# Kernel tuning notes

Measured on AMD Instinct MI355X. Metric: run time of the kernel, lower is better.

Reference implementation:

```python
import jax, jax.numpy as jnp
import numpy as np

N = 50000        # node_num
E = 1600000      # num edges (avg degree 32)
IN_DIM = 128
OUT_DIM = 64
SLOPE = 0.1      # leaky relu slope_ratio
EPS = 1e-12


def setup_inputs() -> dict:
    key = jax.random.key(0)
    k0, k1, k2, k3 = jax.random.split(key, 4)
    x = jax.random.normal(k0, (N, IN_DIM), dtype=jnp.float32)
    edge_index = jax.random.randint(k1, (2, E), 0, N, dtype=jnp.int64)
    # Linear(in_dim, out_dim) params
    W = jax.random.normal(k2, (OUT_DIM, IN_DIM), dtype=jnp.float32) * (1.0 / np.sqrt(IN_DIM))
    b = jnp.zeros((OUT_DIM,), dtype=jnp.float32)
    # attention vector a: [2*out_dim, 1], kaiming-normal-ish init
    a = jax.random.normal(k3, (2 * OUT_DIM, 1), dtype=jnp.float32) * np.sqrt(2.0 / (2 * OUT_DIM))
    return {"x": x, "edge_index": edge_index, "W": W, "b": b, "a": a}


def reference(x, edge_index, W, b, a):
    # new_embeddings = Linear(x)
    new = x @ W.T + b                          # [N, OUT_DIM]
    src = edge_index[0]
    dst = edge_index[1]
    # cat(new[src], new[dst]) @ a  ==  new[src]@a_src + new[dst]@a_dst (avoids [E, 2*OUT] intermediate)
    a_src = a[:OUT_DIM, 0]                     # [OUT_DIM]
    a_dst = a[OUT_DIM:, 0]                     # [OUT_DIM]
    score = new[src] @ a_src + new[dst] @ a_dst  # [E]
    e = jnp.exp(jax.nn.leaky_relu(score, SLOPE))  # [E]
    # spmm(A, ones) -> per-row sum of edge weights; spmm(A, new) -> weighted aggregation
    row_sum = jax.ops.segment_sum(e, src, num_segments=N)                 # [N]
    results = jax.ops.segment_sum(e[:, None] * new[dst], src, num_segments=N)  # [N, OUT_DIM]
    return results / (row_sum[:, None] + EPS)
```

## Files before the change

kernel.cpp:

```cpp
#include <hip/hip_runtime.h>
#include <hip/hip_bf16.h>

#define NN    50000
#define EE    1600000
#define IND   128
#define OUTD  64
#define SLOPE 0.1f

#define BSH    5
#define BW     32
#define NB     1564
#define NFINE  1568
#define CAP    1408
#define CAPT   6
#define CSH    8
#define NC     196
#define CAP1   8832
#define NBLK1  500
#define CHUNK1 (EE / NBLK1)
#define NSPLIT 4
#define SCAP   (CAP1 / NSPLIT)
#define LTILE  64
#define NLIN   782

typedef __attribute__((ext_vector_type(8))) short short8;
typedef __attribute__((ext_vector_type(4))) float float4v;

union SMem {
    struct {
        ushort xs[64 * 136];
        ushort wt[64 * 136];
        float  newt[64 * 68];
    } lin;
    int h[NC];
};

__global__ __launch_bounds__(256) void fused_lincoarse_kernel(
    const float* __restrict__ x, const float* __restrict__ W,
    const float* __restrict__ bias, const float* __restrict__ a,
    const int* __restrict__ ei, int* __restrict__ gcur1,
    unsigned* __restrict__ ebuf1,
    ushort* __restrict__ nbuf2, float* __restrict__ s_src, float* __restrict__ s_dst)
{
    __shared__ SMem sm;
    const int tid = threadIdx.x;

    if (blockIdx.x < NBLK1) {
        int* h = sm.h;
        for (int i = tid; i < NC; i += 256) h[i] = 0;
        __syncthreads();
        const int base = blockIdx.x * CHUNK1;
        const int4* s4p = (const int4*)(ei + base);
        int4 sst[4];
        #pragma unroll
        for (int k = 0; k < 4; ++k) {
            int i = tid + k * 256;
            if (i < CHUNK1 / 4) {
                int4 s4 = s4p[i];
                sst[k] = s4;
                atomicAdd(&h[s4.x >> CSH], 1);
                atomicAdd(&h[s4.y >> CSH], 1);
                atomicAdd(&h[s4.z >> CSH], 1);
                atomicAdd(&h[s4.w >> CSH], 1);
            }
        }
        __syncthreads();
        for (int i = tid; i < NC; i += 256) {
            int c = h[i];
            if (c) h[i] = i * CAP1 + atomicAdd(&gcur1[i * 16], c);
        }
        __syncthreads();
        const int4* d4p = (const int4*)(ei + EE + base);
        #pragma unroll
        for (int k = 0; k < 4; ++k) {
            int i = tid + k * 256;
            if (i < CHUNK1 / 4) {
                int4 s4 = sst[k];
                int4 d4 = d4p[i];
                int p0 = atomicAdd(&h[s4.x >> CSH], 1);
                int p1 = atomicAdd(&h[s4.y >> CSH], 1);
                int p2 = atomicAdd(&h[s4.z >> CSH], 1);
                int p3 = atomicAdd(&h[s4.w >> CSH], 1);
                ebuf1[p0] = ((unsigned)(s4.x & 255) << 16) | (unsigned)d4.x;
                ebuf1[p1] = ((unsigned)(s4.y & 255) << 16) | (unsigned)d4.y;
                ebuf1[p2] = ((unsigned)(s4.z & 255) << 16) | (unsigned)d4.z;
                ebuf1[p3] = ((unsigned)(s4.w & 255) << 16) | (unsigned)d4.w;
            }
        }
        return;
    }

    const int node0 = (blockIdx.x - NBLK1) * LTILE;
    const float4* W4 = (const float4*)W;
    #pragma unroll
    for (int i = 0; i < 8; ++i) {
        int idx = tid + i * 256;
        float4 wv = W4[idx];
        int n = idx >> 5, k = (idx & 31) * 4;
        ushort4 pk; __hip_bfloat16 h;
        h = __float2bfloat16(wv.x); pk.x = *(ushort*)&h;
        h = __float2bfloat16(wv.y); pk.y = *(ushort*)&h;
        h = __float2bfloat16(wv.z); pk.z = *(ushort*)&h;
        h = __float2bfloat16(wv.w); pk.w = *(ushort*)&h;
        *(ushort4*)&sm.lin.wt[n * 136 + k] = pk;
    }
    const float4* x4 = (const float4*)x;
    #pragma unroll
    for (int i = 0; i < 8; ++i) {
        int idx = tid + i * 256;
        int r = idx >> 5, cc = (idx & 31) * 4;
        int gr = node0 + r; if (gr >= NN) gr = NN - 1;
        float4 xv = x4[(size_t)gr * 32 + (idx & 31)];
        ushort4 pk; __hip_bfloat16 h;
        h = __float2bfloat16(xv.x); pk.x = *(ushort*)&h;
        h = __float2bfloat16(xv.y); pk.y = *(ushort*)&h;
        h = __float2bfloat16(xv.z); pk.z = *(ushort*)&h;
        h = __float2bfloat16(xv.w); pk.w = *(ushort*)&h;
        *(ushort4*)&sm.lin.xs[r * 136 + cc] = pk;
    }
    __syncthreads();

    const int w    = tid >> 6;
    const int lane = tid & 63;
    const int q    = lane >> 4;
    const int m16  = lane & 15;
    const float bv = bias[w * 16 + m16];
    #pragma unroll
    for (int t = 0; t < 4; ++t) {
        float4v acc = {0.f, 0.f, 0.f, 0.f};
        #pragma unroll
        for (int kk = 0; kk < IND; kk += 32) {
            short8 af = *(const short8*)&sm.lin.xs[(t * 16 + m16) * 136 + kk + q * 8];
            short8 bf = *(const short8*)&sm.lin.wt[(w * 16 + m16) * 136 + kk + q * 8];
            acc = __builtin_amdgcn_mfma_f32_16x16x32_bf16(af, bf, acc, 0, 0, 0);
        }
        #pragma unroll
        for (int r = 0; r < 4; ++r)
            sm.lin.newt[(t * 16 + q * 4 + r) * 68 + w * 16 + m16] = acc[r] + bv;
    }
    __syncthreads();

    const int jg = tid & 15;
    const int j0 = jg * 4;
    const float a0s = a[j0],        a1s = a[j0 + 1],
                a2s = a[j0 + 2],    a3s = a[j0 + 3];
    const float a0d = a[OUTD + j0],     a1d = a[OUTD + j0 + 1],
                a2d = a[OUTD + j0 + 2], a3d = a[OUTD + j0 + 3];
    #pragma unroll
    for (int t = 0; t < 4; ++t) {
        const int nl = t * 16 + (tid >> 4);
        const int n = node0 + nl;
        float4 va = *(const float4*)&sm.lin.newt[nl * 68 + j0];
        if (n < NN) {
            ushort4 pk; __hip_bfloat16 h;
            h = __float2bfloat16(va.x); pk.x = *(ushort*)&h;
            h = __float2bfloat16(va.y); pk.y = *(ushort*)&h;
            h = __float2bfloat16(va.z); pk.z = *(ushort*)&h;
            h = __float2bfloat16(va.w); pk.w = *(ushort*)&h;
            *(ushort4*)&nbuf2[(size_t)n * OUTD + j0] = pk;
        }
        float ss = va.x * a0s + va.y * a1s + va.z * a2s + va.w * a3s;
        float sd = va.x * a0d + va.y * a1d + va.z * a2d + va.w * a3d;
        #pragma unroll
        for (int m = 1; m < 16; m <<= 1) {
            ss += __shfl_xor(ss, m, 64);
            sd += __shfl_xor(sd, m, 64);
        }
        if (jg == 0 && n < NN) { s_src[n] = ss; s_dst[n] = sd; }
    }
}

__global__ __launch_bounds__(256) void finebin_kernel(
    const unsigned* __restrict__ ebuf1, const int* __restrict__ gcur1,
    int* __restrict__ gcur2, unsigned* __restrict__ ebuf2)
{
    __shared__ unsigned stage[SCAP];
    __shared__ int h[8], lofs[8], grun[8], cur[8];
    const int tid = threadIdx.x;
    const int c   = blockIdx.x >> 2;
    const int sp  = blockIdx.x & 3;
    const int cnt1 = gcur1[c * 16];
    const int seg  = (cnt1 + NSPLIT - 1) / NSPLIT;
    const int lo   = sp * seg;
    const int m    = max(0, min(cnt1, lo + seg) - lo);
    if (tid < 8) h[tid] = 0;
    __syncthreads();
    const unsigned* eb = ebuf1 + (size_t)c * CAP1 + lo;
    for (int i = tid; i < m; i += 256)
        atomicAdd(&h[eb[i] >> 21], 1);
    __syncthreads();
    if (tid == 0) {
        int run = 0;
        #pragma unroll
        for (int f = 0; f < 8; ++f) { lofs[f] = run; run += h[f]; }
    }
    __syncthreads();
    if (tid < 8) {
        cur[tid]  = lofs[tid];
        grun[tid] = atomicAdd(&gcur2[(c * 8 + tid) * 16], h[tid]);
    }
    __syncthreads();
    for (int i = tid; i < m; i += 256) {
        unsigned e = eb[i];
        int pos = atomicAdd(&cur[e >> 21], 1);
        stage[pos] = (((e >> 16) & 31u) << 16) | (e & 0xFFFFu);
    }
    __syncthreads();
    #pragma unroll 1
    for (int f = 0; f < 8; ++f) {
        const int cf = h[f];
        unsigned* dst = ebuf2 + (size_t)(c * 8 + f) * CAP + grun[f];
        const unsigned* sp2 = stage + lofs[f];
        for (int i = tid; i < cf; i += 256) dst[i] = sp2[i];
    }
}

__global__ __launch_bounds__(256) void aggregate_kernel(
    const unsigned* __restrict__ ebuf, const int* __restrict__ gcur,
    const ushort* __restrict__ nbuf2,
    const float* __restrict__ s_src, const float* __restrict__ s_dst,
    float* __restrict__ out)
{
    __shared__ uint2 pairs[CAP];
    __shared__ float ssL[BW];
    __shared__ int cntL[BW], ofs[BW], cur[BW];
    const int tid  = threadIdx.x;
    const int wid  = tid >> 6;
    const int lane = tid & 63;
    const int b    = blockIdx.x;
    const int n0   = b << BSH;
    const uint2* __restrict__ nbufq = (const uint2*)nbuf2;

    if (tid < BW) {
        int n = n0 + tid;
        ssL[tid]  = (n < NN) ? s_src[n] : 0.f;
        cntL[tid] = 0;
    }
    __syncthreads();

    const int cnt = gcur[b * 16];
    const unsigned* eb = ebuf + (size_t)b * CAP;

    unsigned er[CAPT]; float evr[CAPT];
    #pragma unroll
    for (int k = 0; k < CAPT; ++k) {
        int i = tid + k * 256;
        if (i < cnt) {
            unsigned e = eb[i];
            er[k] = e;
            int d  = e & 0xFFFFu;
            int ln = e >> 16;
            float sc = ssL[ln] + s_dst[d];
            float lr = sc > 0.f ? sc : SLOPE * sc;
            evr[k] = __expf(lr);
            atomicAdd(&cntL[ln], 1);
        }
    }
    __syncthreads();

    if (wid == 0) {
        int c = (lane < BW) ? cntL[lane] : 0;
        int sc = c;
        #pragma unroll
        for (int m = 1; m < BW; m <<= 1) {
            int v = __shfl_up(sc, m, 64);
            if (lane >= m) sc += v;
        }
        if (lane < BW) { ofs[lane] = sc - c; cur[lane] = sc - c; }
    }
    __syncthreads();

    #pragma unroll
    for (int k = 0; k < CAPT; ++k) {
        int i = tid + k * 256;
        if (i < cnt) {
            int ln = er[k] >> 16;
            int pos = atomicAdd(&cur[ln], 1);
            pairs[pos] = make_uint2(er[k] & 0xFFFFu, __float_as_uint(evr[k]));
        }
    }
    __syncthreads();

    const int e16 = lane >> 4;
    const int c16 = lane & 15;

    #pragma unroll 1
    for (int t = 0; t < BW / 4; ++t) {
        const int ln  = wid * (BW / 4) + t;
        const int beg = ofs[ln];
        const int len = cntL[ln];

        float a0 = 0.f, a1 = 0.f, a2 = 0.f, a3 = 0.f, es = 0.f;
        int j = 0;
        for (; j + 32 <= len; j += 32) {
            uint2 pA = pairs[beg + j + 0  + e16];
            uint2 pB = pairs[beg + j + 4  + e16];
            uint2 pC = pairs[beg + j + 8  + e16];
            uint2 pD = pairs[beg + j + 12 + e16];
            uint2 pE = pairs[beg + j + 16 + e16];
            uint2 pF = pairs[beg + j + 20 + e16];
            uint2 pG = pairs[beg + j + 24 + e16];
            uint2 pH = pairs[beg + j + 28 + e16];
            uint2 gA = nbufq[pA.x * 16 + c16];
            uint2 gB = nbufq[pB.x * 16 + c16];
            uint2 gC = nbufq[pC.x * 16 + c16];
            uint2 gD = nbufq[pD.x * 16 + c16];
            uint2 gE = nbufq[pE.x * 16 + c16];
            uint2 gF = nbufq[pF.x * 16 + c16];
            uint2 gG = nbufq[pG.x * 16 + c16];
            uint2 gH = nbufq[pH.x * 16 + c16];
            float fA = __uint_as_float(pA.y), fB = __uint_as_float(pB.y);
            float fC = __uint_as_float(pC.y), fD = __uint_as_float(pD.y);
            float fE = __uint_as_float(pE.y), fF = __uint_as_float(pF.y);
            float fG = __uint_as_float(pG.y), fH = __uint_as_float(pH.y);
            es += (fA + fB + fC + fD) + (fE + fF + fG + fH);
            a0 = fmaf(fA, __uint_as_float(gA.x << 16), a0);
            a1 = fmaf(fA, __uint_as_float(gA.x & 0xFFFF0000u), a1);
            a2 = fmaf(fA, __uint_as_float(gA.y << 16), a2);
            a3 = fmaf(fA, __uint_as_float(gA.y & 0xFFFF0000u), a3);
            a0 = fmaf(fB, __uint_as_float(gB.x << 16), a0);
            a1 = fmaf(fB, __uint_as_float(gB.x & 0xFFFF0000u), a1);
            a2 = fmaf(fB, __uint_as_float(gB.y << 16), a2);
            a3 = fmaf(fB, __uint_as_float(gB.y & 0xFFFF0000u), a3);
            a0 = fmaf(fC, __uint_as_float(gC.x << 16), a0);
            a1 = fmaf(fC, __uint_as_float(gC.x & 0xFFFF0000u), a1);
            a2 = fmaf(fC, __uint_as_float(gC.y << 16), a2);
            a3 = fmaf(fC, __uint_as_float(gC.y & 0xFFFF0000u), a3);
            a0 = fmaf(fD, __uint_as_float(gD.x << 16), a0);
            a1 = fmaf(fD, __uint_as_float(gD.x & 0xFFFF0000u), a1);
            a2 = fmaf(fD, __uint_as_float(gD.y << 16), a2);
            a3 = fmaf(fD, __uint_as_float(gD.y & 0xFFFF0000u), a3);
            a0 = fmaf(fE, __uint_as_float(gE.x << 16), a0);
            a1 = fmaf(fE, __uint_as_float(gE.x & 0xFFFF0000u), a1);
            a2 = fmaf(fE, __uint_as_float(gE.y << 16), a2);
            a3 = fmaf(fE, __uint_as_float(gE.y & 0xFFFF0000u), a3);
            a0 = fmaf(fF, __uint_as_float(gF.x << 16), a0);
            a1 = fmaf(fF, __uint_as_float(gF.x & 0xFFFF0000u), a1);
            a2 = fmaf(fF, __uint_as_float(gF.y << 16), a2);
            a3 = fmaf(fF, __uint_as_float(gF.y & 0xFFFF0000u), a3);
            a0 = fmaf(fG, __uint_as_float(gG.x << 16), a0);
            a1 = fmaf(fG, __uint_as_float(gG.x & 0xFFFF0000u), a1);
            a2 = fmaf(fG, __uint_as_float(gG.y << 16), a2);
            a3 = fmaf(fG, __uint_as_float(gG.y & 0xFFFF0000u), a3);
            a0 = fmaf(fH, __uint_as_float(gH.x << 16), a0);
            a1 = fmaf(fH, __uint_as_float(gH.x & 0xFFFF0000u), a1);
            a2 = fmaf(fH, __uint_as_float(gH.y << 16), a2);
            a3 = fmaf(fH, __uint_as_float(gH.y & 0xFFFF0000u), a3);
        }
        for (; j + 16 <= len; j += 16) {
            uint2 pA = pairs[beg + j + 0  + e16];
            uint2 pB = pairs[beg + j + 4  + e16];
            uint2 pC = pairs[beg + j + 8  + e16];
            uint2 pD = pairs[beg + j + 12 + e16];
            uint2 gA = nbufq[pA.x * 16 + c16];
            uint2 gB = nbufq[pB.x * 16 + c16];
            uint2 gC = nbufq[pC.x * 16 + c16];
            uint2 gD = nbufq[pD.x * 16 + c16];
            float fA = __uint_as_float(pA.y), fB = __uint_as_float(pB.y);
            float fC = __uint_as_float(pC.y), fD = __uint_as_float(pD.y);
            es += fA + fB + fC + fD;
            a0 = fmaf(fA, __uint_as_float(gA.x << 16), a0);
            a1 = fmaf(fA, __uint_as_float(gA.x & 0xFFFF0000u), a1);
            a2 = fmaf(fA, __uint_as_float(gA.y << 16), a2);
            a3 = fmaf(fA, __uint_as_float(gA.y & 0xFFFF0000u), a3);
            a0 = fmaf(fB, __uint_as_float(gB.x << 16), a0);
            a1 = fmaf(fB, __uint_as_float(gB.x & 0xFFFF0000u), a1);
            a2 = fmaf(fB, __uint_as_float(gB.y << 16), a2);
            a3 = fmaf(fB, __uint_as_float(gB.y & 0xFFFF0000u), a3);
            a0 = fmaf(fC, __uint_as_float(gC.x << 16), a0);
            a1 = fmaf(fC, __uint_as_float(gC.x & 0xFFFF0000u), a1);
            a2 = fmaf(fC, __uint_as_float(gC.y << 16), a2);
            a3 = fmaf(fC, __uint_as_float(gC.y & 0xFFFF0000u), a3);
            a0 = fmaf(fD, __uint_as_float(gD.x << 16), a0);
            a1 = fmaf(fD, __uint_as_float(gD.x & 0xFFFF0000u), a1);
            a2 = fmaf(fD, __uint_as_float(gD.y << 16), a2);
            a3 = fmaf(fD, __uint_as_float(gD.y & 0xFFFF0000u), a3);
        }
        for (; j < len; j += 4) {
            int idx = j + e16;
            uint2 p = pairs[beg + min(idx, len - 1)];
            float f = (idx < len) ? __uint_as_float(p.y) : 0.f;
            uint2 g = nbufq[p.x * 16 + c16];
            es += f;
            a0 = fmaf(f, __uint_as_float(g.x << 16), a0);
            a1 = fmaf(f, __uint_as_float(g.x & 0xFFFF0000u), a1);
            a2 = fmaf(f, __uint_as_float(g.y << 16), a2);
            a3 = fmaf(f, __uint_as_float(g.y & 0xFFFF0000u), a3);
        }
        es += __shfl_xor(es, 16, 64); es += __shfl_xor(es, 32, 64);
        a0 += __shfl_xor(a0, 16, 64); a0 += __shfl_xor(a0, 32, 64);
        a1 += __shfl_xor(a1, 16, 64); a1 += __shfl_xor(a1, 32, 64);
        a2 += __shfl_xor(a2, 16, 64); a2 += __shfl_xor(a2, 32, 64);
        a3 += __shfl_xor(a3, 16, 64); a3 += __shfl_xor(a3, 32, 64);
        const int n = n0 + ln;
        if (e16 == 0 && n < NN) {
            float inv = 1.f / (es + 1e-12f);
            float4 o = make_float4(a0 * inv, a1 * inv, a2 * inv, a3 * inv);
            *(float4*)&out[(size_t)n * OUTD + c16 * 4] = o;
        }
    }
}

extern "C" void kernel_launch(void* const* d_in, const int* in_sizes, int n_in,
                              void* d_out, int out_size, void* d_ws, size_t ws_size,
                              hipStream_t stream) {
    const float* x  = (const float*)d_in[0];
    const int*   ei = (const int*)d_in[1];
    const float* W  = (const float*)d_in[2];
    const float* b  = (const float*)d_in[3];
    const float* a  = (const float*)d_in[4];
    float* out = (float*)d_out;

    ushort*   nbuf2 = (ushort*)d_ws;
    float*    s_src = (float*)(nbuf2 + (size_t)NN * OUTD);
    float*    s_dst = s_src + NN;
    int*      gcur1 = (int*)(s_dst + NN);
    int*      gcur2 = gcur1 + NC * 16;
    unsigned* ebuf1 = (unsigned*)(gcur2 + NFINE * 16);
    unsigned* ebuf2 = ebuf1 + (size_t)NC * CAP1;

    hipMemsetAsync(gcur1, 0, (NC + NFINE) * 16 * sizeof(int), stream);
    fused_lincoarse_kernel<<<NBLK1 + NLIN, 256, 0, stream>>>(
        x, W, b, a, ei, gcur1, ebuf1, nbuf2, s_src, s_dst);
    finebin_kernel<<<NC * NSPLIT, 256, 0, stream>>>(ebuf1, gcur1, gcur2, ebuf2);
    aggregate_kernel<<<NB, 256, 0, stream>>>(ebuf2, gcur2, nbuf2, s_src, s_dst, out);
    aggregate_kernel<<<NB, 256, 0, stream>>>(ebuf2, gcur2, nbuf2, s_src, s_dst, out);
}
```

Measured before the change: 180.1 us.

## Drop duplicate aggregate launch, ballot-based finebin binning, packed FMA, smaller linear tiles

The host no longer launches the aggregate kernel twice, which removes a full redundant pass. Finebin replaces per-element shared atomics with wave ballots and popcounts, so each wave does one atomic per bin, and it keeps edges in registers between the count and scatter passes. Aggregation accumulates with float2 elementwise FMA, which can map to packed FMA instructions. The linear tile shrinks to 32 rows so the grid has more blocks, at the cost of reloading W more often. The register staging assumes a segment holds at most KST*256 edges; larger segments would be silently dropped.

```diff
diff --git a/kernel.cpp b/kernel.cpp
--- a/kernel.cpp
+++ b/kernel.cpp
@@ -20,17 +20,19 @@
 #define CHUNK1 (EE / NBLK1)
 #define NSPLIT 4
 #define SCAP   (CAP1 / NSPLIT)
-#define LTILE  64
-#define NLIN   782
+#define KST    9
+#define LTILE  32
+#define NLIN   1563
 
 typedef __attribute__((ext_vector_type(8))) short short8;
 typedef __attribute__((ext_vector_type(4))) float float4v;
+typedef __attribute__((ext_vector_type(2))) float float2v;
 
 union SMem {
     struct {
-        ushort xs[64 * 136];
+        ushort xs[32 * 136];
         ushort wt[64 * 136];
-        float  newt[64 * 68];
+        float  newt[32 * 68];
     } lin;
     int h[NC];
 };
@@ -106,7 +108,7 @@
     }
     const float4* x4 = (const float4*)x;
     #pragma unroll
-    for (int i = 0; i < 8; ++i) {
+    for (int i = 0; i < 4; ++i) {
         int idx = tid + i * 256;
         int r = idx >> 5, cc = (idx & 31) * 4;
         int gr = node0 + r; if (gr >= NN) gr = NN - 1;
@@ -126,7 +128,7 @@
     const int m16  = lane & 15;
     const float bv = bias[w * 16 + m16];
     #pragma unroll
-    for (int t = 0; t < 4; ++t) {
+    for (int t = 0; t < 2; ++t) {
         float4v acc = {0.f, 0.f, 0.f, 0.f};
         #pragma unroll
         for (int kk = 0; kk < IND; kk += 32) {
@@ -147,7 +149,7 @@
     const float a0d = a[OUTD + j0],     a1d = a[OUTD + j0 + 1],
                 a2d = a[OUTD + j0 + 2], a3d = a[OUTD + j0 + 3];
     #pragma unroll
-    for (int t = 0; t < 4; ++t) {
+    for (int t = 0; t < 2; ++t) {
         const int nl = t * 16 + (tid >> 4);
         const int n = node0 + nl;
         float4 va = *(const float4*)&sm.lin.newt[nl * 68 + j0];
@@ -176,7 +178,9 @@
 {
     __shared__ unsigned stage[SCAP];
     __shared__ int h[8], lofs[8], grun[8], cur[8];
-    const int tid = threadIdx.x;
+    const int tid  = threadIdx.x;
+    const int lane = tid & 63;
+    const unsigned long long ltmask = ((unsigned long long)1 << lane) - 1;
     const int c   = blockIdx.x >> 2;
     const int sp  = blockIdx.x & 3;
     const int cnt1 = gcur1[c * 16];
@@ -186,8 +190,27 @@
     if (tid < 8) h[tid] = 0;
     __syncthreads();
     const unsigned* eb = ebuf1 + (size_t)c * CAP1 + lo;
-    for (int i = tid; i < m; i += 256)
-        atomicAdd(&h[eb[i] >> 21], 1);
+
+    unsigned est[KST];
+    #pragma unroll
+    for (int k = 0; k < KST; ++k) {
+        int i = tid + k * 256;
+        bool act = i < m;
+        unsigned e = act ? eb[i] : 0u;
+        est[k] = e;
+        unsigned bin = e >> 21;
+        unsigned long long b0 = __ballot(act && (bin & 1));
+        unsigned long long b1 = __ballot(act && (bin & 2));
+        unsigned long long b2 = __ballot(act && (bin & 4));
+        unsigned long long ba = __ballot(act);
+        if (lane < 8) {
+            unsigned long long mk = ((lane & 1) ? b0 : ~b0)
+                                  & ((lane & 2) ? b1 : ~b1)
+                                  & ((lane & 4) ? b2 : ~b2) & ba;
+            int cc = __popcll(mk);
+            if (cc) atomicAdd(&h[lane], cc);
+        }
+    }
     __syncthreads();
     if (tid == 0) {
         int run = 0;
@@ -200,10 +223,30 @@
         grun[tid] = atomicAdd(&gcur2[(c * 8 + tid) * 16], h[tid]);
     }
     __syncthreads();
-    for (int i = tid; i < m; i += 256) {
-        unsigned e = eb[i];
-        int pos = atomicAdd(&cur[e >> 21], 1);
-        stage[pos] = (((e >> 16) & 31u) << 16) | (e & 0xFFFFu);
+    #pragma unroll
+    for (int k = 0; k < KST; ++k) {
+        int i = tid + k * 256;
+        bool act = i < m;
+        unsigned e = est[k];
+        unsigned bin = e >> 21;
+        unsigned long long b0 = __ballot(act && (bin & 1));
+        unsigned long long b1 = __ballot(act && (bin & 2));
+        unsigned long long b2 = __ballot(act && (bin & 4));
+        unsigned long long ba = __ballot(act);
+        int base = 0;
+        if (lane < 8) {
+            unsigned long long mk = ((lane & 1) ? b0 : ~b0)
+                                  & ((lane & 2) ? b1 : ~b1)
+                                  & ((lane & 4) ? b2 : ~b2) & ba;
+            int cc = __popcll(mk);
+            if (cc) base = atomicAdd(&cur[lane], cc);
+        }
+        base = __shfl(base, (int)bin, 64);
+        unsigned long long my = ((bin & 1) ? b0 : ~b0)
+                              & ((bin & 2) ? b1 : ~b1)
+                              & ((bin & 4) ? b2 : ~b2) & ba;
+        int rank = __popcll(my & ltmask);
+        if (act) stage[base + rank] = (((e >> 16) & 31u) << 16) | (e & 0xFFFFu);
     }
     __syncthreads();
     #pragma unroll 1
@@ -214,6 +257,16 @@
         for (int i = tid; i < cf; i += 256) dst[i] = sp2[i];
     }
 }
+
+#define ACC2(fsc, g) do {                                                    \
+    float2v lo_ = { __uint_as_float((g).x << 16),                            \
+                    __uint_as_float((g).x & 0xFFFF0000u) };                  \
+    float2v hi_ = { __uint_as_float((g).y << 16),                            \
+                    __uint_as_float((g).y & 0xFFFF0000u) };                  \
+    float2v fv_ = { (fsc), (fsc) };                                          \
+    acc01 = __builtin_elementwise_fma(fv_, lo_, acc01);                      \
+    acc23 = __builtin_elementwise_fma(fv_, hi_, acc23);                      \
+} while (0)
 
 __global__ __launch_bounds__(256) void aggregate_kernel(
     const unsigned* __restrict__ ebuf, const int* __restrict__ gcur,
@@ -290,7 +343,8 @@
         const int beg = ofs[ln];
         const int len = cntL[ln];
 
-        float a0 = 0.f, a1 = 0.f, a2 = 0.f, a3 = 0.f, es = 0.f;
+        float2v acc01 = {0.f, 0.f}, acc23 = {0.f, 0.f};
+        float es = 0.f;
         int j = 0;
         for (; j + 32 <= len; j += 32) {
             uint2 pA = pairs[beg + j + 0  + e16];
@@ -314,38 +368,8 @@
             float fE = __uint_as_float(pE.y), fF = __uint_as_float(pF.y);
             float fG = __uint_as_float(pG.y), fH = __uint_as_float(pH.y);
             es += (fA + fB + fC + fD) + (fE + fF + fG + fH);
-            a0 = fmaf(fA, __uint_as_float(gA.x << 16), a0);
-            a1 = fmaf(fA, __uint_as_float(gA.x & 0xFFFF0000u), a1);
-            a2 = fmaf(fA, __uint_as_float(gA.y << 16), a2);
-            a3 = fmaf(fA, __uint_as_float(gA.y & 0xFFFF0000u), a3);
-            a0 = fmaf(fB, __uint_as_float(gB.x << 16), a0);
-            a1 = fmaf(fB, __uint_as_float(gB.x & 0xFFFF0000u), a1);
-            a2 = fmaf(fB, __uint_as_float(gB.y << 16), a2);
-            a3 = fmaf(fB, __uint_as_float(gB.y & 0xFFFF0000u), a3);
-            a0 = fmaf(fC, __uint_as_float(gC.x << 16), a0);
-            a1 = fmaf(fC, __uint_as_float(gC.x & 0xFFFF0000u), a1);
-            a2 = fmaf(fC, __uint_as_float(gC.y << 16), a2);
-            a3 = fmaf(fC, __uint_as_float(gC.y & 0xFFFF0000u), a3);
-            a0 = fmaf(fD, __uint_as_float(gD.x << 16), a0);
-            a1 = fmaf(fD, __uint_as_float(gD.x & 0xFFFF0000u), a1);
-            a2 = fmaf(fD, __uint_as_float(gD.y << 16), a2);
-            a3 = fmaf(fD, __uint_as_float(gD.y & 0xFFFF0000u), a3);
-            a0 = fmaf(fE, __uint_as_float(gE.x << 16), a0);
-            a1 = fmaf(fE, __uint_as_float(gE.x & 0xFFFF0000u), a1);
-            a2 = fmaf(fE, __uint_as_float(gE.y << 16), a2);
-            a3 = fmaf(fE, __uint_as_float(gE.y & 0xFFFF0000u), a3);
-            a0 = fmaf(fF, __uint_as_float(gF.x << 16), a0);
-            a1 = fmaf(fF, __uint_as_float(gF.x & 0xFFFF0000u), a1);
-            a2 = fmaf(fF, __uint_as_float(gF.y << 16), a2);
-            a3 = fmaf(fF, __uint_as_float(gF.y & 0xFFFF0000u), a3);
-            a0 = fmaf(fG, __uint_as_float(gG.x << 16), a0);
-            a1 = fmaf(fG, __uint_as_float(gG.x & 0xFFFF0000u), a1);
-            a2 = fmaf(fG, __uint_as_float(gG.y << 16), a2);
-            a3 = fmaf(fG, __uint_as_float(gG.y & 0xFFFF0000u), a3);
-            a0 = fmaf(fH, __uint_as_float(gH.x << 16), a0);
-            a1 = fmaf(fH, __uint_as_float(gH.x & 0xFFFF0000u), a1);
-            a2 = fmaf(fH, __uint_as_float(gH.y << 16), a2);
-            a3 = fmaf(fH, __uint_as_float(gH.y & 0xFFFF0000u), a3);
+            ACC2(fA, gA); ACC2(fB, gB); ACC2(fC, gC); ACC2(fD, gD);
+            ACC2(fE, gE); ACC2(fF, gF); ACC2(fG, gG); ACC2(fH, gH);
         }
         for (; j + 16 <= len; j += 16) {
             uint2 pA = pairs[beg + j + 0  + e16];
@@ -359,22 +383,7 @@
             float fA = __uint_as_float(pA.y), fB = __uint_as_float(pB.y);
             float fC = __uint_as_float(pC.y), fD = __uint_as_float(pD.y);
             es += fA + fB + fC + fD;
-            a0 = fmaf(fA, __uint_as_float(gA.x << 16), a0);
-            a1 = fmaf(fA, __uint_as_float(gA.x & 0xFFFF0000u), a1);
-            a2 = fmaf(fA, __uint_as_float(gA.y << 16), a2);
-            a3 = fmaf(fA, __uint_as_float(gA.y & 0xFFFF0000u), a3);
-            a0 = fmaf(fB, __uint_as_float(gB.x << 16), a0);
-            a1 = fmaf(fB, __uint_as_float(gB.x & 0xFFFF0000u), a1);
-            a2 = fmaf(fB, __uint_as_float(gB.y << 16), a2);
-            a3 = fmaf(fB, __uint_as_float(gB.y & 0xFFFF0000u), a3);
-            a0 = fmaf(fC, __uint_as_float(gC.x << 16), a0);
-            a1 = fmaf(fC, __uint_as_float(gC.x & 0xFFFF0000u), a1);
-            a2 = fmaf(fC, __uint_as_float(gC.y << 16), a2);
-            a3 = fmaf(fC, __uint_as_float(gC.y & 0xFFFF0000u), a3);
-            a0 = fmaf(fD, __uint_as_float(gD.x << 16), a0);
-            a1 = fmaf(fD, __uint_as_float(gD.x & 0xFFFF0000u), a1);
-            a2 = fmaf(fD, __uint_as_float(gD.y << 16), a2);
-            a3 = fmaf(fD, __uint_as_float(gD.y & 0xFFFF0000u), a3);
+            ACC2(fA, gA); ACC2(fB, gB); ACC2(fC, gC); ACC2(fD, gD);
         }
         for (; j < len; j += 4) {
             int idx = j + e16;
@@ -382,11 +391,9 @@
             float f = (idx < len) ? __uint_as_float(p.y) : 0.f;
             uint2 g = nbufq[p.x * 16 + c16];
             es += f;
-            a0 = fmaf(f, __uint_as_float(g.x << 16), a0);
-            a1 = fmaf(f, __uint_as_float(g.x & 0xFFFF0000u), a1);
-            a2 = fmaf(f, __uint_as_float(g.y << 16), a2);
-            a3 = fmaf(f, __uint_as_float(g.y & 0xFFFF0000u), a3);
-        }
+            ACC2(f, g);
+        }
+        float a0 = acc01.x, a1 = acc01.y, a2 = acc23.x, a3 = acc23.y;
         es += __shfl_xor(es, 16, 64); es += __shfl_xor(es, 32, 64);
         a0 += __shfl_xor(a0, 16, 64); a0 += __shfl_xor(a0, 32, 64);
         a1 += __shfl_xor(a1, 16, 64); a1 += __shfl_xor(a1, 32, 64);
@@ -424,5 +431,4 @@
         x, W, b, a, ei, gcur1, ebuf1, nbuf2, s_src, s_dst);
     finebin_kernel<<<NC * NSPLIT, 256, 0, stream>>>(ebuf1, gcur1, gcur2, ebuf2);
     aggregate_kernel<<<NB, 256, 0, stream>>>(ebuf2, gcur2, nbuf2, s_src, s_dst, out);
-    aggregate_kernel<<<NB, 256, 0, stream>>>(ebuf2, gcur2, nbuf2, s_src, s_dst, out);
 }
```

New measurement: 148.9 us. -17.3%, faster.
